# Optimization experiments

Measured on AMD Instinct MI355X. Metric: run time of the kernel, lower is better.

The kernel has to match this reference:

```python
import jax, jax.numpy as jnp
import numpy as np


def setup_inputs() -> dict:
    key = jax.random.key(0)
    ks = jax.random.split(key, 7)
    bs, win_len, num_obj, d = 4, 64, 36, 2048
    s = 1.0 / np.sqrt(d)
    return {
        "region_feats": jax.random.normal(ks[0], (bs, win_len, num_obj, d), jnp.float32),
        "Wq": jax.random.normal(ks[1], (d, d), jnp.float32) * s,
        "bq": jax.random.normal(ks[2], (d,), jnp.float32) * 0.01,
        "Wk": jax.random.normal(ks[3], (d, d), jnp.float32) * s,
        "bk": jax.random.normal(ks[4], (d,), jnp.float32) * 0.01,
        "Wu": jax.random.normal(ks[5], (d, 1024), jnp.float32) * s,
        "bu": jax.random.normal(ks[6], (1024,), jnp.float32) * 0.01,
    }


def reference(region_feats, Wq, bq, Wk, bk, Wu, bu):
    bs, win_len, num_obj, d = region_feats.shape
    feats = region_feats.reshape(bs, win_len * num_obj, d)  # [b, n, d]
    q = feats @ Wq + bq                                     # [b, n, d]
    k = feats @ Wk + bk                                     # [b, n, d]
    adj = jnp.einsum('bnd,bmd->bnm', q, k)                  # unscaled QK^T, [b, n, n]
    adj_norm = jax.nn.softmax(adj, axis=-1)
    v = feats @ Wu + bu                                     # [b, n, 1024]
    out = jnp.einsum('bnm,bmv->bnv', adj_norm, v)
    return out.reshape(bs, win_len, num_obj, -1)
```

## Files before the change

### kernel.cpp

```cpp
#include <hip/hip_runtime.h>


typedef unsigned short u16;
typedef unsigned int   u32;
typedef signed char    i8;
typedef _Float16 f16;
typedef f16    f16x8 __attribute__((ext_vector_type(8)));
typedef float  f32x4 __attribute__((ext_vector_type(4)));
typedef int    i32x4 __attribute__((ext_vector_type(4)));
typedef u32    u32x4 __attribute__((ext_vector_type(4)));
typedef u16    u16x4 __attribute__((ext_vector_type(4)));

#define WAIT_VM8   0x0F78
#define WAIT_VM4   0x0F74
#define WAIT_VM0   0x0F70
#define WAIT_LGKM0 0xC07F

__device__ __forceinline__ void gload16(const void* g, void* l) {
    __builtin_amdgcn_global_load_lds(
        (const __attribute__((address_space(1))) unsigned int*)g,
        (__attribute__((address_space(3))) unsigned int*)l, 16, 0, 0);
}

__device__ __forceinline__ void tile_swizzle(int& tx, int& ty) {
    const int gx = gridDim.x, gy = gridDim.y;
    const int lin = blockIdx.y * gx + blockIdx.x;
    const int G = 4;
    const int gid = lin / (G * gx);
    const int g0 = gid * G;
    const int gh = min(G, gy - g0);
    const int rem = lin - gid * (G * gx);
    ty = g0 + rem % gh;
    tx = rem / gh;
}

__device__ __forceinline__ void digits256(float v, float s, i8& d1, i8& d0) {
    float f = fminf(fmaxf(v * s, -32600.0f), 32600.0f);
    int r = __float2int_rn(f);
    int a1 = (r + 128) >> 8;
    int a0 = r - (a1 << 8);
    d1 = (i8)a1;
    d0 = (i8)a0;
}

__global__ __launch_bounds__(256) void quantFc_k(const float* __restrict__ F,
                                                 const float* __restrict__ u,
                                                 u16* __restrict__ F16,
                                                 i8* __restrict__ hi,
                                                 i8* __restrict__ lo,
                                                 float* __restrict__ c) {
    const long row = blockIdx.x;
    const int tid = threadIdx.x;
    const float* fr = F + row * 2048;
    float dot = 0.f;
    #pragma unroll
    for (int t = 0; t < 8; ++t) {
        const int i = t * 256 + tid;
        const float v = fr[i];
        F16[row * 2048 + i] = __builtin_bit_cast(u16, (f16)v);
        i8 d1, d0;
        digits256(v, 5440.0f, d1, d0);
        hi[row * 2048 + i] = d1;
        lo[row * 2048 + i] = d0;
        dot += v * u[i];
    }
    #pragma unroll
    for (int off = 32; off >= 1; off >>= 1) dot += __shfl_down(dot, off);
    __shared__ float red[4];
    if ((tid & 63) == 0) red[tid >> 6] = dot;
    __syncthreads();
    if (tid == 0) c[row] = red[0] + red[1] + red[2] + red[3];
}

__global__ __launch_bounds__(256) void quantW_k(const float* __restrict__ x,
                                                i8* __restrict__ hi,
                                                i8* __restrict__ lo, long n) {
    long i = (long)blockIdx.x * 256 + threadIdx.x;
    if (i < n) {
        i8 d1, d0;
        digits256(x[i], 261120.0f, d1, d0);
        hi[i] = d1;
        lo[i] = d0;
    }
}

__global__ __launch_bounds__(256) void wut_k(const float* __restrict__ Wu,
                                             u16* __restrict__ WuT) {
    __shared__ float t[32][33];
    const int bx = blockIdx.x * 32;
    const int by = blockIdx.y * 32;
    const int lx = threadIdx.x, ly = threadIdx.y;
    #pragma unroll
    for (int dy = 0; dy < 32; dy += 8)
        t[ly + dy][lx] = Wu[(long)(by + ly + dy) * 1024 + bx + lx];
    __syncthreads();
    #pragma unroll
    for (int dy = 0; dy < 32; dy += 8)
        WuT[(long)(bx + ly + dy) * 2048 + by + lx] =
            __builtin_bit_cast(u16, (f16)t[lx][ly + dy]);
}

__global__ __launch_bounds__(256) void gemv_k(const float* __restrict__ A,
                                              const float* __restrict__ x,
                                              float* __restrict__ y, int ncols) {
    const long row = blockIdx.x;
    const float* ar = A + row * (long)ncols;
    float s = 0.f;
    for (int i = threadIdx.x; i < ncols; i += 256) s += ar[i] * x[i];
    #pragma unroll
    for (int off = 32; off >= 1; off >>= 1) s += __shfl_down(s, off);
    __shared__ float red[4];
    if ((threadIdx.x & 63) == 0) red[threadIdx.x >> 6] = s;
    __syncthreads();
    if (threadIdx.x == 0) y[row] = red[0] + red[1] + red[2] + red[3];
}

template <int EPI>
__global__ __launch_bounds__(256, 2) void gemm_i8(
    const i8* __restrict__ Ah, const i8* __restrict__ Al,
    const i8* __restrict__ Bh, const i8* __restrict__ Bl,
    i8* __restrict__ Qh, i8* __restrict__ Ql, float* __restrict__ Cf,
    float oscale, int N, int K, long strA, long strB, long strC) {
    __shared__ __align__(16) i8 lds[2][32768];

    const int tid  = threadIdx.x;
    const int lane = tid & 63;
    const int wv   = tid >> 6;
    const int wm   = wv >> 1, wn = wv & 1;
    const int l16  = lane & 15, kq = lane >> 4;
    const int z    = blockIdx.z;
    int tx, ty;
    tile_swizzle(tx, ty);
    const long rowBase = (long)ty * 128;
    const long colBase = (long)tx * 128;

    const i8* pAh = Ah + (long)z * strA;
    const i8* pAl = Al + (long)z * strA;
    const i8* pBh = Bh + (long)z * strB;
    const i8* pBl = Bl + (long)z * strB;

    const int l4r = lane >> 2, l4c = lane & 3;
    int rin[2], kqw[2];
    u32 voffA[2], voffB[2];
    int ldsoff[2];
    #pragma unroll
    for (int h = 0; h < 2; ++h) {
        rin[h] = h * 64 + wv * 16 + l4r;
        kqw[h] = (l4c - (rin[h] >> 1)) & 3;
        voffA[h] = (u32)((rowBase + rin[h]) * (long)K) + kqw[h] * 16;
        voffB[h] = (u32)((colBase + rin[h]) * (long)K) + kqw[h] * 16;
        ldsoff[h] = (h * 64 + wv * 16) * 64;
    }

    int aoff[4], boff[4];
    #pragma unroll
    for (int i = 0; i < 4; ++i) {
        const int rA = wm * 64 + i * 16 + l16;
        aoff[i] = rA * 64 + ((kq + (rA >> 1)) & 3) * 16;
        const int rB = wn * 64 + i * 16 + l16;
        boff[i] = rB * 64 + ((kq + (rB >> 1)) & 3) * 16;
    }

    const i32x4 izero = {0, 0, 0, 0};
    i32x4 ahh[4][4], acx[4][4], all_[4][4];
    #pragma unroll
    for (int i = 0; i < 4; ++i)
        #pragma unroll
        for (int j = 0; j < 4; ++j) { ahh[i][j] = izero; acx[i][j] = izero; all_[i][j] = izero; }

    const int nk = K >> 6;

    #pragma unroll
    for (int h = 0; h < 2; ++h) {
        gload16(pAh + voffA[h], &lds[0][0]     + ldsoff[h]);
        gload16(pAl + voffA[h], &lds[0][8192]  + ldsoff[h]);
        gload16(pBh + voffB[h], &lds[0][16384] + ldsoff[h]);
        gload16(pBl + voffB[h], &lds[0][24576] + ldsoff[h]);
    }

    for (int kt = 0; kt < nk; ++kt) {
        const int cur = kt & 1;
        if (kt + 1 < nk) {
            const long ko = (long)(kt + 1) * 64;
            i8* nb = lds[1 - cur];
            #pragma unroll
            for (int h = 0; h < 2; ++h) {
                gload16(pAh + voffA[h] + ko, nb         + ldsoff[h]);
                gload16(pAl + voffA[h] + ko, nb + 8192  + ldsoff[h]);
                gload16(pBh + voffB[h] + ko, nb + 16384 + ldsoff[h]);
                gload16(pBl + voffB[h] + ko, nb + 24576 + ldsoff[h]);
            }
            __builtin_amdgcn_s_waitcnt(WAIT_VM8);
        } else {
            __builtin_amdgcn_s_waitcnt(WAIT_VM0);
        }
        __builtin_amdgcn_s_barrier();

        const i8* base = lds[cur];
        i32x4 fbh[4], fbl[4];
        #pragma unroll
        for (int j = 0; j < 4; ++j) {
            fbh[j] = *(const i32x4*)(base + 16384 + boff[j]);
            fbl[j] = *(const i32x4*)(base + 24576 + boff[j]);
        }
        #pragma unroll
        for (int i = 0; i < 4; ++i) {
            i32x4 fah = *(const i32x4*)(base + aoff[i]);
            i32x4 fal = *(const i32x4*)(base + 8192 + aoff[i]);
            #pragma unroll
            for (int j = 0; j < 4; ++j) {
                ahh[i][j]  = __builtin_amdgcn_mfma_i32_16x16x64_i8(fah, fbh[j], ahh[i][j], 0, 0, 0);
                acx[i][j]  = __builtin_amdgcn_mfma_i32_16x16x64_i8(fah, fbl[j], acx[i][j], 0, 0, 0);
                acx[i][j]  = __builtin_amdgcn_mfma_i32_16x16x64_i8(fal, fbh[j], acx[i][j], 0, 0, 0);
                all_[i][j] = __builtin_amdgcn_mfma_i32_16x16x64_i8(fal, fbl[j], all_[i][j], 0, 0, 0);
            }
        }
        __builtin_amdgcn_s_waitcnt(WAIT_LGKM0);
        __builtin_amdgcn_s_barrier();
    }

    #pragma unroll
    for (int i = 0; i < 4; ++i) {
        const long gr0 = rowBase + wm * 64 + i * 16 + kq * 4;
        #pragma unroll
        for (int j = 0; j < 4; ++j) {
            const long gc = colBase + wn * 64 + j * 16 + l16;
            #pragma unroll
            for (int r = 0; r < 4; ++r) {
                const float comb = 65536.0f * (float)ahh[i][j][r] +
                                     256.0f * (float)acx[i][j][r] +
                                             (float)all_[i][j][r];
                const long o = (gr0 + r) * (long)N + gc;
                if constexpr (EPI == 0) {
                    i8 d1, d0;
                    digits256(comb, oscale, d1, d0);
                    Qh[o] = d1;
                    Ql[o] = d0;
                } else {
                    Cf[(long)z * strC + o] = comb * oscale;
                }
            }
        }
    }
}

template <int EPI>
__global__ __launch_bounds__(256, 3) void gemm_f16(
    const u16* __restrict__ A, const u16* __restrict__ B,
    u16* __restrict__ Ch, float* __restrict__ Cf,
    const float* __restrict__ bias,
    int N, int K, long strA, long strB, long strC) {
    __shared__ __align__(16) i8 lds[2][16384];

    const int tid  = threadIdx.x;
    const int lane = tid & 63;
    const int wv   = tid >> 6;
    const int wm   = wv >> 1, wn = wv & 1;
    const int l16  = lane & 15, kq = lane >> 4;
    const int z    = blockIdx.z;
    int tx, ty;
    tile_swizzle(tx, ty);
    const long rowBase = (long)ty * 128;
    const long colBase = (long)tx * 128;

    const u16* pA = A + (long)z * strA;
    const u16* pB = B + (long)z * strB;

    const int l4r = lane >> 2, l4c = lane & 3;
    u32 voffA[2], voffB[2];
    int ldsoff[2];
    #pragma unroll
    for (int h = 0; h < 2; ++h) {
        const int rin = h * 64 + wv * 16 + l4r;
        const int kw = (l4c - (rin >> 1)) & 3;
        voffA[h] = (u32)((rowBase + rin) * (long)K) + kw * 8;
        voffB[h] = (u32)((colBase + rin) * (long)K) + kw * 8;
        ldsoff[h] = (h * 64 + wv * 16) * 64;
    }
    int aoff[4], boff[4];
    #pragma unroll
    for (int i = 0; i < 4; ++i) {
        const int rA = wm * 64 + i * 16 + l16;
        aoff[i] = rA * 64 + ((kq + (rA >> 1)) & 3) * 16;
        const int rB = wn * 64 + i * 16 + l16;
        boff[i] = rB * 64 + ((kq + (rB >> 1)) & 3) * 16;
    }

    const f32x4 vzero = {0.f, 0.f, 0.f, 0.f};
    f32x4 acc[4][4];
    #pragma unroll
    for (int i = 0; i < 4; ++i)
        #pragma unroll
        for (int j = 0; j < 4; ++j) acc[i][j] = vzero;

    const int nk = K >> 5;

    #pragma unroll
    for (int h = 0; h < 2; ++h) {
        gload16(pA + voffA[h], &lds[0][0]    + ldsoff[h]);
        gload16(pB + voffB[h], &lds[0][8192] + ldsoff[h]);
    }

    for (int kt = 0; kt < nk; ++kt) {
        const int cur = kt & 1;
        if (kt + 1 < nk) {
            const long ko = (long)(kt + 1) * 32;
            i8* nb = lds[1 - cur];
            #pragma unroll
            for (int h = 0; h < 2; ++h) {
                gload16(pA + voffA[h] + ko, nb        + ldsoff[h]);
                gload16(pB + voffB[h] + ko, nb + 8192 + ldsoff[h]);
            }
            __builtin_amdgcn_s_waitcnt(WAIT_VM4);
        } else {
            __builtin_amdgcn_s_waitcnt(WAIT_VM0);
        }
        __builtin_amdgcn_s_barrier();

        const i8* base = lds[cur];
        f16x8 fa[4];
        #pragma unroll
        for (int i = 0; i < 4; ++i)
            fa[i] = __builtin_bit_cast(f16x8, *(const u32x4*)(base + aoff[i]));
        #pragma unroll
        for (int j = 0; j < 4; ++j) {
            f16x8 fb = __builtin_bit_cast(f16x8, *(const u32x4*)(base + 8192 + boff[j]));
            #pragma unroll
            for (int i = 0; i < 4; ++i)
                acc[i][j] = __builtin_amdgcn_mfma_f32_16x16x32_f16(fa[i], fb, acc[i][j], 0, 0, 0);
        }
        __builtin_amdgcn_s_waitcnt(WAIT_LGKM0);
        __builtin_amdgcn_s_barrier();
    }

    #pragma unroll
    for (int i = 0; i < 4; ++i) {
        const long gr0 = rowBase + wm * 64 + i * 16 + kq * 4;
        #pragma unroll
        for (int j = 0; j < 4; ++j) {
            const long gc = colBase + wn * 64 + j * 16 + l16;
            f32x4 a = acc[i][j];
            if constexpr (EPI == 2) {
                const int b  = (int)(gr0 / 2304);
                const int n0 = (int)(gr0 - (long)b * 2304);
                u16x4 o4;
                #pragma unroll
                for (int r = 0; r < 4; ++r) o4[r] = __builtin_bit_cast(u16, (f16)a[r]);
                *(u16x4*)&Ch[(long)b * (1024L * 2304) + gc * 2304 + n0] = o4;
            } else {
                float* C = Cf + (long)z * strC;
                const float bv = bias[gc];
                #pragma unroll
                for (int r = 0; r < 4; ++r) C[(gr0 + r) * (long)N + gc] = a[r] + bv;
            }
        }
    }
}

__global__ __launch_bounds__(256) void softmax_k(const float* __restrict__ adj,
                                                 const float* __restrict__ c,
                                                 u16* __restrict__ P) {
    const int n = 2304;
    const int row = blockIdx.x, b = blockIdx.y;
    const int tid = threadIdx.x;
    const float* ar = adj + ((long)b * n + row) * (long)n;
    const float* cb = c + (long)b * n;
    u16* pr = P + ((long)b * n + row) * (long)n;

    float v[9];
    float mx = -3.0e38f;
    #pragma unroll
    for (int t = 0; t < 9; ++t) {
        const int i = t * 256 + tid;
        const float x = ar[i] + cb[i];
        v[t] = x;
        mx = fmaxf(mx, x);
    }
    #pragma unroll
    for (int off = 32; off >= 1; off >>= 1) mx = fmaxf(mx, __shfl_down(mx, off));
    __shared__ float red[4];
    if ((tid & 63) == 0) red[tid >> 6] = mx;
    __syncthreads();
    mx = fmaxf(fmaxf(red[0], red[1]), fmaxf(red[2], red[3]));

    float s = 0.f;
    #pragma unroll
    for (int t = 0; t < 9; ++t) {
        const float e = __expf(v[t] - mx);
        v[t] = e;
        s += e;
    }
    #pragma unroll
    for (int off = 32; off >= 1; off >>= 1) s += __shfl_down(s, off);
    __shared__ float red2[4];
    if ((tid & 63) == 0) red2[tid >> 6] = s;
    __syncthreads();
    s = red2[0] + red2[1] + red2[2] + red2[3];
    const float inv = 1.0f / s;
    #pragma unroll
    for (int t = 0; t < 9; ++t)
        pr[t * 256 + tid] = __builtin_bit_cast(u16, (f16)(v[t] * inv));
}

extern "C" void kernel_launch(void* const* d_in, const int* in_sizes, int n_in,
                              void* d_out, int out_size, void* d_ws, size_t ws_size,
                              hipStream_t stream) {
    (void)in_sizes; (void)n_in; (void)out_size; (void)ws_size;
    const float* F  = (const float*)d_in[0];
    const float* Wq = (const float*)d_in[1];
    const float* bq = (const float*)d_in[2];
    const float* Wk = (const float*)d_in[3];
    const float* Wu = (const float*)d_in[5];
    const float* bu = (const float*)d_in[6];
    float* out = (float*)d_out;

    char* ws = (char*)d_ws;
    const long o_F16  = 0L;
    const long o_Fh8  = 37748736L;
    const long o_Fl8  = 56623104L;
    const long o_Sh8  = 75497472L;
    const long o_Sl8  = 94371840L;
    const long o_adj  = 113246208L;
    const long o_P    = 198180864L;
    const long o_vT   = 240648192L;
    const long o_WuT  = 259522560L;
    const long o_Wqh  = 263716864L;
    const long o_Wql  = 267911168L;
    const long o_Wkh  = 272105472L;
    const long o_Wkl  = 276299776L;
    const long o_Mth  = 280494080L;
    const long o_Mtl  = 284688384L;
    const long o_u    = 288882688L;
    const long o_c    = 288890880L;

    u16* F16 = (u16*)(ws + o_F16);
    i8*  Fh8 = (i8*)(ws + o_Fh8);   i8* Fl8 = (i8*)(ws + o_Fl8);
    i8*  Sh8 = (i8*)(ws + o_Sh8);   i8* Sl8 = (i8*)(ws + o_Sl8);
    float* adj = (float*)(ws + o_adj);
    u16* P   = (u16*)(ws + o_P);
    u16* vT  = (u16*)(ws + o_vT);
    u16* WuT = (u16*)(ws + o_WuT);
    i8*  Wqh = (i8*)(ws + o_Wqh);   i8* Wql = (i8*)(ws + o_Wql);
    i8*  Wkh = (i8*)(ws + o_Wkh);   i8* Wkl = (i8*)(ws + o_Wkl);
    i8*  Mth = (i8*)(ws + o_Mth);   i8* Mtl = (i8*)(ws + o_Mtl);
    float* u = (float*)(ws + o_u);
    float* c = (float*)(ws + o_c);

    gemv_k<<<2048, 256, 0, stream>>>(Wk, bq, u, 2048);
    quantFc_k<<<9216, 256, 0, stream>>>(F, u, F16, Fh8, Fl8, c);
    quantW_k<<<16384, 256, 0, stream>>>(Wq, Wqh, Wql, 4194304L);
    quantW_k<<<16384, 256, 0, stream>>>(Wk, Wkh, Wkl, 4194304L);
    wut_k<<<dim3(32, 64, 1), dim3(32, 8, 1), 0, stream>>>(Wu, WuT);

    gemm_i8<0><<<dim3(16, 16, 1), 256, 0, stream>>>(
        Wkh, Wkl, Wqh, Wql, Mth, Mtl, nullptr,
        3.8296569e-06f, 2048, 2048, 0L, 0L, 0L);

    gemm_i8<0><<<dim3(16, 72, 1), 256, 0, stream>>>(
        Fh8, Fl8, Mth, Mtl, Sh8, Sl8, nullptr,
        3.8296569e-06f, 2048, 2048, 0L, 0L, 0L);

    gemm_i8<1><<<dim3(18, 18, 4), 256, 0, stream>>>(
        Sh8, Sl8, Fh8, Fl8, nullptr, nullptr, adj,
        3.3791083e-08f, 2304, 2048,
        2304L * 2048, 2304L * 2048, 2304L * 2304);

    softmax_k<<<dim3(2304, 4, 1), 256, 0, stream>>>(adj, c, P);

    gemm_f16<2><<<dim3(8, 72, 1), 256, 0, stream>>>(
        F16, WuT, vT, nullptr, nullptr, 1024, 2048, 0L, 0L, 0L);

    gemm_f16<3><<<dim3(8, 18, 4), 256, 0, stream>>>(
        P, vT, nullptr, out, bu, 1024, 2304,
        2304L * 2304, 1024L * 2304, 2304L * 1024);
}
```

Before: 649.6 us.

## Merge prep kernels and co-schedule independent GEMMs in shared launches

Combines the gemv, weight quantization and Wu transpose into one launch. The Wk·Wq product GEMM now shares a launch with the feature quantization, and the S GEMM shares a launch with the V projection GEMM. This cuts launch count and lets independent work fill idle CUs, especially for the small 256-tile Mt GEMM and the 576-tile v GEMM. The risk is that the fused kernels take the larger LDS size and occupancy bound, so the f16 GEMM runs at 2 blocks per CU instead of 3. Inside the merged launches the tile swizzle is also dropped in favour of linear block indexing.

New measurement: 632.3 us. 2.7% less time.

```diff
diff --git a/kernel.cpp b/kernel.cpp
--- a/kernel.cpp
+++ b/kernel.cpp
@@ -43,94 +43,18 @@
     d0 = (i8)a0;
 }
 
-__global__ __launch_bounds__(256) void quantFc_k(const float* __restrict__ F,
-                                                 const float* __restrict__ u,
-                                                 u16* __restrict__ F16,
-                                                 i8* __restrict__ hi,
-                                                 i8* __restrict__ lo,
-                                                 float* __restrict__ c) {
-    const long row = blockIdx.x;
-    const int tid = threadIdx.x;
-    const float* fr = F + row * 2048;
-    float dot = 0.f;
-    #pragma unroll
-    for (int t = 0; t < 8; ++t) {
-        const int i = t * 256 + tid;
-        const float v = fr[i];
-        F16[row * 2048 + i] = __builtin_bit_cast(u16, (f16)v);
-        i8 d1, d0;
-        digits256(v, 5440.0f, d1, d0);
-        hi[row * 2048 + i] = d1;
-        lo[row * 2048 + i] = d0;
-        dot += v * u[i];
-    }
-    #pragma unroll
-    for (int off = 32; off >= 1; off >>= 1) dot += __shfl_down(dot, off);
-    __shared__ float red[4];
-    if ((tid & 63) == 0) red[tid >> 6] = dot;
-    __syncthreads();
-    if (tid == 0) c[row] = red[0] + red[1] + red[2] + red[3];
-}
-
-__global__ __launch_bounds__(256) void quantW_k(const float* __restrict__ x,
-                                                i8* __restrict__ hi,
-                                                i8* __restrict__ lo, long n) {
-    long i = (long)blockIdx.x * 256 + threadIdx.x;
-    if (i < n) {
-        i8 d1, d0;
-        digits256(x[i], 261120.0f, d1, d0);
-        hi[i] = d1;
-        lo[i] = d0;
-    }
-}
-
-__global__ __launch_bounds__(256) void wut_k(const float* __restrict__ Wu,
-                                             u16* __restrict__ WuT) {
-    __shared__ float t[32][33];
-    const int bx = blockIdx.x * 32;
-    const int by = blockIdx.y * 32;
-    const int lx = threadIdx.x, ly = threadIdx.y;
-    #pragma unroll
-    for (int dy = 0; dy < 32; dy += 8)
-        t[ly + dy][lx] = Wu[(long)(by + ly + dy) * 1024 + bx + lx];
-    __syncthreads();
-    #pragma unroll
-    for (int dy = 0; dy < 32; dy += 8)
-        WuT[(long)(bx + ly + dy) * 2048 + by + lx] =
-            __builtin_bit_cast(u16, (f16)t[lx][ly + dy]);
-}
-
-__global__ __launch_bounds__(256) void gemv_k(const float* __restrict__ A,
-                                              const float* __restrict__ x,
-                                              float* __restrict__ y, int ncols) {
-    const long row = blockIdx.x;
-    const float* ar = A + row * (long)ncols;
-    float s = 0.f;
-    for (int i = threadIdx.x; i < ncols; i += 256) s += ar[i] * x[i];
-    #pragma unroll
-    for (int off = 32; off >= 1; off >>= 1) s += __shfl_down(s, off);
-    __shared__ float red[4];
-    if ((threadIdx.x & 63) == 0) red[threadIdx.x >> 6] = s;
-    __syncthreads();
-    if (threadIdx.x == 0) y[row] = red[0] + red[1] + red[2] + red[3];
-}
-
 template <int EPI>
-__global__ __launch_bounds__(256, 2) void gemm_i8(
+__device__ __forceinline__ void gemm_i8_body(
+    i8* ldsb, int tx, int ty, int z,
     const i8* __restrict__ Ah, const i8* __restrict__ Al,
     const i8* __restrict__ Bh, const i8* __restrict__ Bl,
     i8* __restrict__ Qh, i8* __restrict__ Ql, float* __restrict__ Cf,
     float oscale, int N, int K, long strA, long strB, long strC) {
-    __shared__ __align__(16) i8 lds[2][32768];
-
     const int tid  = threadIdx.x;
     const int lane = tid & 63;
     const int wv   = tid >> 6;
     const int wm   = wv >> 1, wn = wv & 1;
     const int l16  = lane & 15, kq = lane >> 4;
-    const int z    = blockIdx.z;
-    int tx, ty;
-    tile_swizzle(tx, ty);
     const long rowBase = (long)ty * 128;
     const long colBase = (long)tx * 128;
 
@@ -140,15 +64,15 @@
     const i8* pBl = Bl + (long)z * strB;
 
     const int l4r = lane >> 2, l4c = lane & 3;
-    int rin[2], kqw[2];
+    int rin[2];
     u32 voffA[2], voffB[2];
     int ldsoff[2];
     #pragma unroll
     for (int h = 0; h < 2; ++h) {
         rin[h] = h * 64 + wv * 16 + l4r;
-        kqw[h] = (l4c - (rin[h] >> 1)) & 3;
-        voffA[h] = (u32)((rowBase + rin[h]) * (long)K) + kqw[h] * 16;
-        voffB[h] = (u32)((colBase + rin[h]) * (long)K) + kqw[h] * 16;
+        const int kw = (l4c - (rin[h] >> 1)) & 3;
+        voffA[h] = (u32)((rowBase + rin[h]) * (long)K) + kw * 16;
+        voffB[h] = (u32)((colBase + rin[h]) * (long)K) + kw * 16;
         ldsoff[h] = (h * 64 + wv * 16) * 64;
     }
 
@@ -172,17 +96,17 @@
 
     #pragma unroll
     for (int h = 0; h < 2; ++h) {
-        gload16(pAh + voffA[h], &lds[0][0]     + ldsoff[h]);
-        gload16(pAl + voffA[h], &lds[0][8192]  + ldsoff[h]);
-        gload16(pBh + voffB[h], &lds[0][16384] + ldsoff[h]);
-        gload16(pBl + voffB[h], &lds[0][24576] + ldsoff[h]);
+        gload16(pAh + voffA[h], ldsb         + ldsoff[h]);
+        gload16(pAl + voffA[h], ldsb + 8192  + ldsoff[h]);
+        gload16(pBh + voffB[h], ldsb + 16384 + ldsoff[h]);
+        gload16(pBl + voffB[h], ldsb + 24576 + ldsoff[h]);
     }
 
     for (int kt = 0; kt < nk; ++kt) {
         const int cur = kt & 1;
         if (kt + 1 < nk) {
             const long ko = (long)(kt + 1) * 64;
-            i8* nb = lds[1 - cur];
+            i8* nb = ldsb + (1 - cur) * 32768;
             #pragma unroll
             for (int h = 0; h < 2; ++h) {
                 gload16(pAh + voffA[h] + ko, nb         + ldsoff[h]);
@@ -196,7 +120,7 @@
         }
         __builtin_amdgcn_s_barrier();
 
-        const i8* base = lds[cur];
+        const i8* base = ldsb + cur * 32768;
         i32x4 fbh[4], fbl[4];
         #pragma unroll
         for (int j = 0; j < 4; ++j) {
@@ -245,21 +169,17 @@
 }
 
 template <int EPI>
-__global__ __launch_bounds__(256, 3) void gemm_f16(
+__device__ __forceinline__ void gemm_f16_body(
+    i8* ldsb, int tx, int ty, int z,
     const u16* __restrict__ A, const u16* __restrict__ B,
     u16* __restrict__ Ch, float* __restrict__ Cf,
     const float* __restrict__ bias,
     int N, int K, long strA, long strB, long strC) {
-    __shared__ __align__(16) i8 lds[2][16384];
-
     const int tid  = threadIdx.x;
     const int lane = tid & 63;
     const int wv   = tid >> 6;
     const int wm   = wv >> 1, wn = wv & 1;
     const int l16  = lane & 15, kq = lane >> 4;
-    const int z    = blockIdx.z;
-    int tx, ty;
-    tile_swizzle(tx, ty);
     const long rowBase = (long)ty * 128;
     const long colBase = (long)tx * 128;
 
@@ -297,15 +217,15 @@
 
     #pragma unroll
     for (int h = 0; h < 2; ++h) {
-        gload16(pA + voffA[h], &lds[0][0]    + ldsoff[h]);
-        gload16(pB + voffB[h], &lds[0][8192] + ldsoff[h]);
+        gload16(pA + voffA[h], ldsb        + ldsoff[h]);
+        gload16(pB + voffB[h], ldsb + 8192 + ldsoff[h]);
     }
 
     for (int kt = 0; kt < nk; ++kt) {
         const int cur = kt & 1;
         if (kt + 1 < nk) {
             const long ko = (long)(kt + 1) * 32;
-            i8* nb = lds[1 - cur];
+            i8* nb = ldsb + (1 - cur) * 16384;
             #pragma unroll
             for (int h = 0; h < 2; ++h) {
                 gload16(pA + voffA[h] + ko, nb        + ldsoff[h]);
@@ -317,7 +237,7 @@
         }
         __builtin_amdgcn_s_barrier();
 
-        const i8* base = lds[cur];
+        const i8* base = ldsb + cur * 16384;
         f16x8 fa[4];
         #pragma unroll
         for (int i = 0; i < 4; ++i)
@@ -355,6 +275,146 @@
             }
         }
     }
+}
+
+__device__ __forceinline__ void quantFc_body(long row, float* red,
+                                             const float* __restrict__ F,
+                                             const float* __restrict__ u,
+                                             u16* __restrict__ F16,
+                                             i8* __restrict__ hi,
+                                             i8* __restrict__ lo,
+                                             float* __restrict__ c) {
+    const int tid = threadIdx.x;
+    const float* fr = F + row * 2048;
+    float dot = 0.f;
+    #pragma unroll
+    for (int t = 0; t < 8; ++t) {
+        const int i = t * 256 + tid;
+        const float v = fr[i];
+        F16[row * 2048 + i] = __builtin_bit_cast(u16, (f16)v);
+        i8 d1, d0;
+        digits256(v, 5440.0f, d1, d0);
+        hi[row * 2048 + i] = d1;
+        lo[row * 2048 + i] = d0;
+        dot += v * u[i];
+    }
+    #pragma unroll
+    for (int off = 32; off >= 1; off >>= 1) dot += __shfl_down(dot, off);
+    if ((tid & 63) == 0) red[tid >> 6] = dot;
+    __syncthreads();
+    if (tid == 0) c[row] = red[0] + red[1] + red[2] + red[3];
+}
+
+__global__ __launch_bounds__(256) void prep_k(const float* __restrict__ Wk,
+                                              const float* __restrict__ bq,
+                                              float* __restrict__ u,
+                                              const float* __restrict__ Wq,
+                                              i8* __restrict__ Wqh, i8* __restrict__ Wql,
+                                              i8* __restrict__ Wkh, i8* __restrict__ Wkl,
+                                              const float* __restrict__ Wu,
+                                              u16* __restrict__ WuT) {
+    __shared__ __align__(16) float sm[32 * 33];
+    const int tid = threadIdx.x;
+    const int id = blockIdx.x;
+    if (id < 2048) {
+        const float* ar = Wk + (long)id * 2048;
+        float s = 0.f;
+        #pragma unroll
+        for (int t = 0; t < 8; ++t) s += ar[t * 256 + tid] * bq[t * 256 + tid];
+        #pragma unroll
+        for (int off = 32; off >= 1; off >>= 1) s += __shfl_down(s, off);
+        if ((tid & 63) == 0) sm[tid >> 6] = s;
+        __syncthreads();
+        if (tid == 0) u[id] = sm[0] + sm[1] + sm[2] + sm[3];
+    } else if (id < 4096) {
+        const int w  = id - 2048;
+        const int bx = (w & 31) * 32;
+        const int by = (w >> 5) * 32;
+        const int lx = tid & 31, ly = tid >> 5;
+        float (*t)[33] = (float (*)[33])sm;
+        #pragma unroll
+        for (int dy = 0; dy < 32; dy += 8)
+            t[ly + dy][lx] = Wu[(long)(by + ly + dy) * 1024 + bx + lx];
+        __syncthreads();
+        #pragma unroll
+        for (int dy = 0; dy < 32; dy += 8)
+            WuT[(long)(bx + ly + dy) * 2048 + by + lx] =
+                __builtin_bit_cast(u16, (f16)t[lx][ly + dy]);
+    } else {
+        long j = (long)id - 4096;
+        const float* src;
+        i8 *dh, *dl;
+        if (j < 16384) { src = Wq; dh = Wqh; dl = Wql; }
+        else           { j -= 16384; src = Wk; dh = Wkh; dl = Wkl; }
+        const long i = j * 256 + tid;
+        i8 d1, d0;
+        digits256(src[i], 261120.0f, d1, d0);
+        dh[i] = d1;
+        dl[i] = d0;
+    }
+}
+
+__global__ __launch_bounds__(256, 2) void fused_qfc_mt(
+    const float* __restrict__ F, const float* __restrict__ u,
+    u16* __restrict__ F16, i8* __restrict__ Fh, i8* __restrict__ Fl,
+    float* __restrict__ c,
+    const i8* __restrict__ Wqh, const i8* __restrict__ Wql,
+    const i8* __restrict__ Wkh, const i8* __restrict__ Wkl,
+    i8* __restrict__ Mth, i8* __restrict__ Mtl) {
+    __shared__ __align__(16) i8 lds[2][32768];
+    const int b = blockIdx.x;
+    if (b < 256) {
+        gemm_i8_body<0>(&lds[0][0], b & 15, b >> 4, 0,
+                        Wkh, Wkl, Wqh, Wql, Mth, Mtl, nullptr,
+                        3.8296569e-06f, 2048, 2048, 0L, 0L, 0L);
+    } else {
+        quantFc_body((long)b - 256, (float*)&lds[0][0], F, u, F16, Fh, Fl, c);
+    }
+}
+
+__global__ __launch_bounds__(256, 2) void fused_sv(
+    const i8* __restrict__ Fh, const i8* __restrict__ Fl,
+    const i8* __restrict__ Mth, const i8* __restrict__ Mtl,
+    i8* __restrict__ Sh, i8* __restrict__ Sl,
+    const u16* __restrict__ F16, const u16* __restrict__ WuT,
+    u16* __restrict__ vT) {
+    __shared__ __align__(16) i8 lds[2][32768];
+    const int bx = blockIdx.x, by = blockIdx.y;
+    if (bx < 16) {
+        gemm_i8_body<0>(&lds[0][0], bx, by, 0,
+                        Fh, Fl, Mth, Mtl, Sh, Sl, nullptr,
+                        3.8296569e-06f, 2048, 2048, 0L, 0L, 0L);
+    } else {
+        gemm_f16_body<2>(&lds[0][0], bx - 16, by, 0,
+                         F16, WuT, vT, nullptr, nullptr,
+                         1024, 2048, 0L, 0L, 0L);
+    }
+}
+
+template <int EPI>
+__global__ __launch_bounds__(256, 2) void gemm_i8_k(
+    const i8* __restrict__ Ah, const i8* __restrict__ Al,
+    const i8* __restrict__ Bh, const i8* __restrict__ Bl,
+    i8* __restrict__ Qh, i8* __restrict__ Ql, float* __restrict__ Cf,
+    float oscale, int N, int K, long strA, long strB, long strC) {
+    __shared__ __align__(16) i8 lds[2][32768];
+    int tx, ty;
+    tile_swizzle(tx, ty);
+    gemm_i8_body<EPI>(&lds[0][0], tx, ty, blockIdx.z,
+                      Ah, Al, Bh, Bl, Qh, Ql, Cf, oscale, N, K, strA, strB, strC);
+}
+
+template <int EPI>
+__global__ __launch_bounds__(256, 3) void gemm_f16_k(
+    const u16* __restrict__ A, const u16* __restrict__ B,
+    u16* __restrict__ Ch, float* __restrict__ Cf,
+    const float* __restrict__ bias,
+    int N, int K, long strA, long strB, long strC) {
+    __shared__ __align__(16) i8 lds[2][16384];
+    int tx, ty;
+    tile_swizzle(tx, ty);
+    gemm_f16_body<EPI>(&lds[0][0], tx, ty, blockIdx.z,
+                       A, B, Ch, Cf, bias, N, K, strA, strB, strC);
 }
 
 __global__ __launch_bounds__(256) void softmax_k(const float* __restrict__ adj,
@@ -446,31 +506,22 @@
     float* u = (float*)(ws + o_u);
     float* c = (float*)(ws + o_c);
 
-    gemv_k<<<2048, 256, 0, stream>>>(Wk, bq, u, 2048);
-    quantFc_k<<<9216, 256, 0, stream>>>(F, u, F16, Fh8, Fl8, c);
-    quantW_k<<<16384, 256, 0, stream>>>(Wq, Wqh, Wql, 4194304L);
-    quantW_k<<<16384, 256, 0, stream>>>(Wk, Wkh, Wkl, 4194304L);
-    wut_k<<<dim3(32, 64, 1), dim3(32, 8, 1), 0, stream>>>(Wu, WuT);
-
-    gemm_i8<0><<<dim3(16, 16, 1), 256, 0, stream>>>(
-        Wkh, Wkl, Wqh, Wql, Mth, Mtl, nullptr,
-        3.8296569e-06f, 2048, 2048, 0L, 0L, 0L);
-
-    gemm_i8<0><<<dim3(16, 72, 1), 256, 0, stream>>>(
-        Fh8, Fl8, Mth, Mtl, Sh8, Sl8, nullptr,
-        3.8296569e-06f, 2048, 2048, 0L, 0L, 0L);
-
-    gemm_i8<1><<<dim3(18, 18, 4), 256, 0, stream>>>(
+    prep_k<<<36864, 256, 0, stream>>>(Wk, bq, u, Wq, Wqh, Wql, Wkh, Wkl, Wu, WuT);
+
+    fused_qfc_mt<<<9472, 256, 0, stream>>>(F, u, F16, Fh8, Fl8, c,
+                                           Wqh, Wql, Wkh, Wkl, Mth, Mtl);
+
+    fused_sv<<<dim3(24, 72, 1), 256, 0, stream>>>(Fh8, Fl8, Mth, Mtl, Sh8, Sl8,
+                                                  F16, WuT, vT);
+
+    gemm_i8_k<1><<<dim3(18, 18, 4), 256, 0, stream>>>(
         Sh8, Sl8, Fh8, Fl8, nullptr, nullptr, adj,
         3.3791083e-08f, 2304, 2048,
         2304L * 2048, 2304L * 2048, 2304L * 2304);
 
     softmax_k<<<dim3(2304, 4, 1), 256, 0, stream>>>(adj, c, P);
 
-    gemm_f16<2><<<dim3(8, 72, 1), 256, 0, stream>>>(
-        F16, WuT, vT, nullptr, nullptr, 1024, 2048, 0L, 0L, 0L);
-
-    gemm_f16<3><<<dim3(8, 18, 4), 256, 0, stream>>>(
+    gemm_f16_k<3><<<dim3(8, 18, 4), 256, 0, stream>>>(
         P, vT, nullptr, out, bu, 1024, 2304,
         2304L * 2304, 1024L * 2304, 2304L * 1024);
 }
```
